# Kernel optimization log

Hardware: AMD Instinct MI355X
Metric: run time of the kernel (lower is better)

## Reference

```python
import jax, jax.numpy as jnp
import numpy as np

NUM_FREQS = 10
NUM_VOXELS = 512
N_POINTS = 262144
IN_DIM = 3
INPUT_CH = IN_DIM + 2 * NUM_FREQS * IN_DIM  # 63


def posenc(x, num_freqs):
    # NeRF positional encoding: [x, sin(x*2^0), cos(x*2^0), ..., sin(x*2^(F-1)), cos(x*2^(F-1))]
    freqs = (2.0 ** jnp.arange(num_freqs)).astype(x.dtype)           # (F,)
    xf = x[:, None, :] * freqs[None, :, None]                        # (N, F, D)
    sc = jnp.stack([jnp.sin(xf), jnp.cos(xf)], axis=2)               # (N, F, 2, D)
    return jnp.concatenate([x, sc.reshape(x.shape[0], -1)], axis=-1)  # (N, D + 2*F*D)


def setup_inputs() -> dict:
    key = jax.random.key(0)
    k_x, k_w, k_v = jax.random.split(key, 3)
    X = jax.random.normal(k_x, (N_POINTS, IN_DIM), dtype=jnp.float32)
    # linear_mappings reshaped to (3*num_voxels, input_ch), used as Linear weight (no bias)
    W = jax.random.normal(k_w, (3 * NUM_VOXELS, INPUT_CH), dtype=jnp.float32) * 0.02
    row_ids = jnp.arange(N_POINTS, dtype=jnp.int64 if jax.config.jax_enable_x64 else jnp.int32)
    voxel_ids = jax.random.randint(k_v, (N_POINTS,), 0, NUM_VOXELS)
    return {"X": X, "W": W, "row_ids": row_ids, "voxel_ids": voxel_ids}


def reference(X, W, row_ids, voxel_ids):
    encoded_X = posenc(X, NUM_FREQS)                      # (N, 63)
    rgb_clusters = encoded_X @ W.T                        # (N, 3*num_voxels) -- wasteful dense GEMM
    # col_indices per selected row: [3v, 3v+1, 3v+2]
    cols = jnp.stack([3 * voxel_ids, 3 * voxel_ids + 1, 3 * voxel_ids + 2], axis=1)  # (M, 3)
    vals = rgb_clusters[row_ids[:, None], cols]           # (M, 3)
    rgb = jnp.zeros((X.shape[0], 3), dtype=X.dtype)
    rgb = rgb.at[row_ids].set(vals)
    return rgb
```

## Files before the change

### kernel.cpp

```cpp
#include <hip/hip_runtime.h>
#include <math.h>

#define N_POINTS   262144
#define NUM_FREQS  10
#define NUM_VOXELS 512
#define HALF_VOX   256
#define VSTRIDE    200
#define HALF_HALFS (HALF_VOX * VSTRIDE)
#define HALF_F4    (HALF_HALFS / 8)


typedef _Float16 half2v __attribute__((ext_vector_type(2)));

__device__ __forceinline__ half2v u2h(unsigned int u) {
    union { unsigned int u; half2v h; } c; c.u = u; return c.h;
}

__device__ __forceinline__ float dot2acc(half2v a, half2v b, float acc) {
#if __has_builtin(__builtin_amdgcn_fdot2)
    return __builtin_amdgcn_fdot2(a, b, acc, false);
#else
    return acc + (float)a[0] * (float)b[0] + (float)a[1] * (float)b[1];
#endif
}

__device__ __forceinline__ half2v pkrtz(float a, float b) {
#if __has_builtin(__builtin_amdgcn_cvt_pkrtz)
    auto r = __builtin_amdgcn_cvt_pkrtz(a, b);
    union { decltype(r) r_; half2v h; } c; c.r_ = r; return c.h;
#else
    half2v h; h[0] = (_Float16)a; h[1] = (_Float16)b; return h;
#endif
}

__global__ __launch_bounds__(1024) void pack_w(
    const float* __restrict__ W, _Float16* __restrict__ Wp)
{
    const int g  = blockIdx.x * 1024 + threadIdx.x;
    const int v  = g / 50;
    const int p0 = (g - v * 50) * 4;
    union { _Float16 h[4]; float2 f2; } u;
    #pragma unroll
    for (int j = 0; j < 4; ++j) {
        const int p = p0 + j;
        float val = 0.0f;
        if (p < 192) {
            const int row = p >> 6, col = p & 63;
            if (col != 3) {
                const int wc = col - (col >= 4);
                val = W[v * 189 + row * 63 + wc];
            }
        }
        u.h[j] = (_Float16)val;
    }
    _Float16* dst = Wp + (size_t)(v >> 8) * HALF_HALFS
                       + (size_t)(v & 255) * VSTRIDE + p0;
    *reinterpret_cast<float2*>(dst) = u.f2;
}

__global__ __launch_bounds__(1024) void voxlin_lds(
    const float* __restrict__ X,
    const _Float16* __restrict__ Wp,
    const int* __restrict__ row_ids,
    const int* __restrict__ voxel_ids,
    float* __restrict__ out)
{
    __shared__ float4 lwv[HALF_F4];
    _Float16* const lw = (_Float16*)lwv;

    const int t = threadIdx.x;
    const int i = blockIdx.x * 1024 + t;

    const int   v  = voxel_ids[i];
    const float x0 = X[3*i + 0];
    const float x1 = X[3*i + 1];
    const float x2 = X[3*i + 2];
    const int   r  = row_ids[i];

    half2v eh[32];
    eh[0] = pkrtz(x0, x1);
    eh[1] = pkrtz(x2, 0.0f);
    {
        float s0, c0, s1, c1, s2, c2;
        __sincosf(x0, &s0, &c0);
        __sincosf(x1, &s1, &c1);
        __sincosf(x2, &s2, &c2);
        #pragma unroll
        for (int f = 0; f < NUM_FREQS; ++f) {
            const int b = 2 + 3 * f;
            eh[b + 0] = pkrtz(s0, s1);
            eh[b + 1] = pkrtz(s2, c0);
            eh[b + 2] = pkrtz(c1, c2);
            if (f < NUM_FREQS - 1) {
                const float ns0 = 2.0f*s0*c0, nc0 = c0*c0 - s0*s0;
                const float ns1 = 2.0f*s1*c1, nc1 = c1*c1 - s1*s1;
                const float ns2 = 2.0f*s2*c2, nc2 = c2*c2 - s2*s2;
                s0 = ns0; c0 = nc0; s1 = ns1; c1 = nc1; s2 = ns2; c2 = nc2;
            }
        }
    }

    float a0 = 0.0f, a1 = 0.0f, a2 = 0.0f;

    #pragma unroll
    for (int h = 0; h < 2; ++h) {
        const float4* __restrict__ src = (const float4*)Wp + h * HALF_F4;
        #pragma unroll
        for (int j = t; j < HALF_F4; j += 1024)
            lwv[j] = src[j];
        __syncthreads();

        if ((v >> 8) == h) {
            const uint4* __restrict__ wb =
                (const uint4*)lw + (v & (HALF_VOX - 1)) * (VSTRIDE / 8);
            float acc[3];
            #pragma unroll
            for (int rr = 0; rr < 3; ++rr) {
                float a = 0.0f;
                #pragma unroll
                for (int k = 0; k < 8; ++k) {
                    const uint4 q = wb[rr * 8 + k];
                    a = dot2acc(u2h(q.x), eh[4*k + 0], a);
                    a = dot2acc(u2h(q.y), eh[4*k + 1], a);
                    a = dot2acc(u2h(q.z), eh[4*k + 2], a);
                    a = dot2acc(u2h(q.w), eh[4*k + 3], a);
                }
                acc[rr] = a;
            }
            a0 = acc[0]; a1 = acc[1]; a2 = acc[2];
        }
        __syncthreads();
    }

    out[3*r + 0] = a0;
    out[3*r + 1] = a1;
    out[3*r + 2] = a2;
}

__global__ __launch_bounds__(256) void voxlin_fallback(
    const float* __restrict__ X, const float* __restrict__ W,
    const int* __restrict__ row_ids, const int* __restrict__ voxel_ids,
    float* __restrict__ out)
{
    const int i = blockIdx.x * 256 + threadIdx.x;
    if (i >= N_POINTS) return;
    const float x0 = X[3*i], x1 = X[3*i+1], x2 = X[3*i+2];
    const int v = voxel_ids[i];
    const float* __restrict__ w0 = W + v * 189;
    const float* __restrict__ w1 = w0 + 63;
    const float* __restrict__ w2 = w0 + 126;
    float a0 = x0*w0[0] + x1*w0[1] + x2*w0[2];
    float a1 = x0*w1[0] + x1*w1[1] + x2*w1[2];
    float a2 = x0*w2[0] + x1*w2[1] + x2*w2[2];
    float s0, c0, s1, c1, s2, c2;
    __sincosf(x0, &s0, &c0); __sincosf(x1, &s1, &c1); __sincosf(x2, &s2, &c2);
    #pragma unroll
    for (int f = 0; f < NUM_FREQS; ++f) {
        const int b = 3 + 6*f;
        a0 += s0*w0[b] + s1*w0[b+1] + s2*w0[b+2] + c0*w0[b+3] + c1*w0[b+4] + c2*w0[b+5];
        a1 += s0*w1[b] + s1*w1[b+1] + s2*w1[b+2] + c0*w1[b+3] + c1*w1[b+4] + c2*w1[b+5];
        a2 += s0*w2[b] + s1*w2[b+1] + s2*w2[b+2] + c0*w2[b+3] + c1*w2[b+4] + c2*w2[b+5];
        if (f < NUM_FREQS - 1) {
            const float ns0 = 2.0f*s0*c0, nc0 = c0*c0 - s0*s0;
            const float ns1 = 2.0f*s1*c1, nc1 = c1*c1 - s1*s1;
            const float ns2 = 2.0f*s2*c2, nc2 = c2*c2 - s2*s2;
            s0 = ns0; c0 = nc0; s1 = ns1; c1 = nc1; s2 = ns2; c2 = nc2;
        }
    }
    const int rr = row_ids[i];
    out[3*rr] = a0; out[3*rr+1] = a1; out[3*rr+2] = a2;
}

extern "C" void kernel_launch(void* const* d_in, const int* in_sizes, int n_in,
                              void* d_out, int out_size, void* d_ws, size_t ws_size,
                              hipStream_t stream) {
    const float* X         = (const float*)d_in[0];
    const float* W         = (const float*)d_in[1];
    const int*   row_ids   = (const int*)d_in[2];
    const int*   voxel_ids = (const int*)d_in[3];
    float*       out       = (float*)d_out;

    const size_t need = (size_t)2 * HALF_HALFS * sizeof(_Float16);

    if (ws_size >= need) {
        _Float16* Wp = (_Float16*)d_ws;
        pack_w<<<50, 1024, 0, stream>>>(W, Wp);
        voxlin_lds<<<N_POINTS / 1024, 1024, 0, stream>>>(X, Wp, row_ids,
                                                         voxel_ids, out);
    } else {
        voxlin_fallback<<<(N_POINTS + 255) / 256, 256, 0, stream>>>(
            X, W, row_ids, voxel_ids, out);
    }
}
```

Measured before the change: 69.55 us.

## Stage weights per output row with double-buffered LDS and register prefetch

```diff
diff --git a/kernel.cpp b/kernel.cpp
--- a/kernel.cpp
+++ b/kernel.cpp
@@ -4,10 +4,9 @@
 #define N_POINTS   262144
 #define NUM_FREQS  10
 #define NUM_VOXELS 512
-#define HALF_VOX   256
-#define VSTRIDE    200
-#define HALF_HALFS (HALF_VOX * VSTRIDE)
-#define HALF_F4    (HALF_HALFS / 8)
+#define RSTRIDE_H  72
+#define ROW_HALFS  (NUM_VOXELS * RSTRIDE_H)
+#define ROW_F4     (ROW_HALFS / 8)
 
 
 typedef _Float16 half2v __attribute__((ext_vector_type(2)));
@@ -33,49 +32,54 @@
 #endif
 }
 
-__global__ __launch_bounds__(1024) void pack_w(
+__global__ __launch_bounds__(256) void pack_w(
     const float* __restrict__ W, _Float16* __restrict__ Wp)
 {
-    const int g  = blockIdx.x * 1024 + threadIdx.x;
-    const int v  = g / 50;
-    const int p0 = (g - v * 50) * 4;
-    union { _Float16 h[4]; float2 f2; } u;
-    #pragma unroll
-    for (int j = 0; j < 4; ++j) {
-        const int p = p0 + j;
+    const int g   = blockIdx.x * 256 + threadIdx.x;
+    const int v   = g / 27;
+    const int rem = g - v * 27;
+    const int rw  = rem / 9;
+    const int gg  = rem - rw * 9;
+    union { _Float16 h[8]; float4 f4; } u;
+    #pragma unroll
+    for (int j = 0; j < 8; ++j) {
+        const int pc = gg * 8 + j;
         float val = 0.0f;
-        if (p < 192) {
-            const int row = p >> 6, col = p & 63;
-            if (col != 3) {
-                const int wc = col - (col >= 4);
-                val = W[v * 189 + row * 63 + wc];
-            }
+        if (pc < 64 && pc != 3) {
+            const int wc = pc - (pc >= 4);
+            val = W[v * 189 + rw * 63 + wc];
         }
         u.h[j] = (_Float16)val;
     }
-    _Float16* dst = Wp + (size_t)(v >> 8) * HALF_HALFS
-                       + (size_t)(v & 255) * VSTRIDE + p0;
-    *reinterpret_cast<float2*>(dst) = u.f2;
-}
-
-__global__ __launch_bounds__(1024) void voxlin_lds(
+    _Float16* dst = Wp + (size_t)rw * ROW_HALFS + v * RSTRIDE_H + gg * 8;
+    *reinterpret_cast<float4*>(dst) = u.f4;
+}
+
+__global__ __launch_bounds__(1024) void voxlin_rows(
     const float* __restrict__ X,
     const _Float16* __restrict__ Wp,
     const int* __restrict__ row_ids,
     const int* __restrict__ voxel_ids,
     float* __restrict__ out)
 {
-    __shared__ float4 lwv[HALF_F4];
-    _Float16* const lw = (_Float16*)lwv;
+    __shared__ uint4 buf[2][ROW_F4];
 
     const int t = threadIdx.x;
     const int i = blockIdx.x * 1024 + t;
 
-    const int   v  = voxel_ids[i];
-    const float x0 = X[3*i + 0];
-    const float x1 = X[3*i + 1];
-    const float x2 = X[3*i + 2];
-    const int   r  = row_ids[i];
+    const uint4* __restrict__ wsrc = (const uint4*)Wp;
+    uint4 tmp[5];
+    #pragma unroll
+    for (int k = 0; k < 5; ++k) {
+        const int idx = k * 1024 + t;
+        if (idx < ROW_F4) tmp[k] = wsrc[idx];
+    }
+
+    const int   v   = voxel_ids[i];
+    const int   rid = row_ids[i];
+    const float x0  = X[3*i + 0];
+    const float x1  = X[3*i + 1];
+    const float x2  = X[3*i + 2];
 
     half2v eh[32];
     eh[0] = pkrtz(x0, x1);
@@ -100,41 +104,50 @@
         }
     }
 
-    float a0 = 0.0f, a1 = 0.0f, a2 = 0.0f;
-
-    #pragma unroll
-    for (int h = 0; h < 2; ++h) {
-        const float4* __restrict__ src = (const float4*)Wp + h * HALF_F4;
+    #pragma unroll
+    for (int k = 0; k < 5; ++k) {
+        const int idx = k * 1024 + t;
+        if (idx < ROW_F4) buf[0][idx] = tmp[k];
+    }
+    __syncthreads();
+
+    float res[3];
+    #pragma unroll
+    for (int rw = 0; rw < 3; ++rw) {
+        if (rw < 2) {
+            const uint4* __restrict__ src = (const uint4*)Wp + (rw + 1) * ROW_F4;
+            #pragma unroll
+            for (int k = 0; k < 5; ++k) {
+                const int idx = k * 1024 + t;
+                if (idx < ROW_F4) tmp[k] = src[idx];
+            }
+        }
+
+        const uint4* __restrict__ wb = &buf[rw & 1][v * 9];
+        float a = 0.0f;
         #pragma unroll
-        for (int j = t; j < HALF_F4; j += 1024)
-            lwv[j] = src[j];
-        __syncthreads();
-
-        if ((v >> 8) == h) {
-            const uint4* __restrict__ wb =
-                (const uint4*)lw + (v & (HALF_VOX - 1)) * (VSTRIDE / 8);
-            float acc[3];
+        for (int k = 0; k < 8; ++k) {
+            const uint4 q = wb[k];
+            a = dot2acc(u2h(q.x), eh[4*k + 0], a);
+            a = dot2acc(u2h(q.y), eh[4*k + 1], a);
+            a = dot2acc(u2h(q.z), eh[4*k + 2], a);
+            a = dot2acc(u2h(q.w), eh[4*k + 3], a);
+        }
+        res[rw] = a;
+
+        if (rw < 2) {
             #pragma unroll
-            for (int rr = 0; rr < 3; ++rr) {
-                float a = 0.0f;
-                #pragma unroll
-                for (int k = 0; k < 8; ++k) {
-                    const uint4 q = wb[rr * 8 + k];
-                    a = dot2acc(u2h(q.x), eh[4*k + 0], a);
-                    a = dot2acc(u2h(q.y), eh[4*k + 1], a);
-                    a = dot2acc(u2h(q.z), eh[4*k + 2], a);
-                    a = dot2acc(u2h(q.w), eh[4*k + 3], a);
-                }
-                acc[rr] = a;
+            for (int k = 0; k < 5; ++k) {
+                const int idx = k * 1024 + t;
+                if (idx < ROW_F4) buf[(rw + 1) & 1][idx] = tmp[k];
             }
-            a0 = acc[0]; a1 = acc[1]; a2 = acc[2];
-        }
-        __syncthreads();
-    }
-
-    out[3*r + 0] = a0;
-    out[3*r + 1] = a1;
-    out[3*r + 2] = a2;
+            __syncthreads();
+        }
+    }
+
+    out[3*rid + 0] = res[0];
+    out[3*rid + 1] = res[1];
+    out[3*rid + 2] = res[2];
 }
 
 __global__ __launch_bounds__(256) void voxlin_fallback(
@@ -180,13 +193,13 @@
     const int*   voxel_ids = (const int*)d_in[3];
     float*       out       = (float*)d_out;
 
-    const size_t need = (size_t)2 * HALF_HALFS * sizeof(_Float16);
+    const size_t need = (size_t)3 * ROW_HALFS * sizeof(_Float16);
 
     if (ws_size >= need) {
         _Float16* Wp = (_Float16*)d_ws;
-        pack_w<<<50, 1024, 0, stream>>>(W, Wp);
-        voxlin_lds<<<N_POINTS / 1024, 1024, 0, stream>>>(X, Wp, row_ids,
-                                                         voxel_ids, out);
+        pack_w<<<54, 256, 0, stream>>>(W, Wp);
+        voxlin_rows<<<N_POINTS / 1024, 1024, 0, stream>>>(X, Wp, row_ids,
+                                                          voxel_ids, out);
     } else {
         voxlin_fallback<<<(N_POINTS + 255) / 256, 256, 0, stream>>>(
             X, W, row_ids, voxel_ids, out);
```

New measurement: 79.62 us. +14.5%, slower.
